# Performance work log

Hardware: AMD Instinct MI355X
Metric: run time of the kernel (lower is better)

Reference implementation:

```python
import jax, jax.numpy as jnp
import numpy as np

B, S, H, NH = 2, 2048, 2048, 16
HD = H // NH  # 128
NEG = -1e9


def _rope_tables(seq_len, dim, dtype):
    inv_freq = 1.0 / (10000.0 ** (jnp.arange(0, dim, 2, dtype=jnp.float32) / dim))
    t = jnp.arange(seq_len, dtype=jnp.float32)
    freqs = jnp.einsum('i,j->ij', t, inv_freq)          # [S, dim/2]
    emb = jnp.concatenate([freqs, freqs], axis=-1)      # [S, dim]
    return jnp.cos(emb).astype(dtype), jnp.sin(emb).astype(dtype)


def _rotate_half(x):
    x1, x2 = x[..., : x.shape[-1] // 2], x[..., x.shape[-1] // 2:]
    return jnp.concatenate([-x2, x1], axis=-1)


def setup_inputs() -> dict:
    key = jax.random.key(0)
    ks = jax.random.split(key, 5)
    hidden_states = jax.random.normal(ks[0], (B, S, H), dtype=jnp.float32)
    # causal additive mask [B, S, S]
    causal = jnp.where(jnp.tril(jnp.ones((S, S), dtype=bool)), 0.0, NEG).astype(jnp.float32)
    attention_mask = jnp.broadcast_to(causal, (B, S, S))
    sc = 1.0 / np.sqrt(H)
    Wq = jax.random.normal(ks[1], (H, H), dtype=jnp.float32) * sc
    Wk = jax.random.normal(ks[2], (H, H), dtype=jnp.float32) * sc
    Wv = jax.random.normal(ks[3], (H, H), dtype=jnp.float32) * sc
    Wo = jax.random.normal(ks[4], (H, H), dtype=jnp.float32) * sc
    return {"hidden_states": hidden_states, "attention_mask": attention_mask,
            "Wq": Wq, "Wk": Wk, "Wv": Wv, "Wo": Wo}


def reference(hidden_states, attention_mask, Wq, Wk, Wv, Wo):
    bsz, q_len, _ = hidden_states.shape
    dtype = hidden_states.dtype
    # QKV projections (nn.Linear: x @ W.T), split into heads -> [B, NH, S, HD]
    def proj(W):
        return jnp.einsum('bsh,dh->bsd', hidden_states, W).reshape(bsz, q_len, NH, HD).transpose(0, 2, 1, 3)
    q, k, v = proj(Wq), proj(Wk), proj(Wv)
    cos, sin = _rope_tables(q_len, HD, dtype)            # [S, HD]
    q = q * cos + _rotate_half(q) * sin
    k = k * cos + _rotate_half(k) * sin
    scaling = HD ** -0.5
    scores = jnp.einsum('bhqd,bhkd->bhqk', q, k) * scaling
    scores = scores + attention_mask[:, None, :, :]      # broadcast over heads
    attn = jax.nn.softmax(scores.astype(jnp.float32), axis=-1).astype(dtype)
    out = jnp.einsum('bhqk,bhkd->bhqd', attn, v)         # [B, NH, S, HD]
    out = out.transpose(0, 2, 1, 3).reshape(bsz, q_len, H)
    return jnp.einsum('bsh,dh->bsd', out, Wo)
```

## Files before the change

kernel.cpp:

```cpp
#include <hip/hip_runtime.h>
#include <hip/hip_bf16.h>
#include <math.h>

#define B_  2
#define S_  2048
#define H_  2048
#define NH_ 16
#define HD_ 128
#define M_  (B_*S_)

typedef __bf16 bf16_t;
typedef _Float16 f16_t;
typedef __bf16 bf16x8 __attribute__((ext_vector_type(8)));
typedef __bf16 bf16x4 __attribute__((ext_vector_type(4)));
typedef _Float16 f16x4 __attribute__((ext_vector_type(4)));
typedef float  f32x4  __attribute__((ext_vector_type(4)));

__device__ __forceinline__ f32x4 mfma_bf16_32(bf16x8 a, bf16x8 b, f32x4 c) {
  return __builtin_amdgcn_mfma_f32_16x16x32_bf16(a, b, c, 0, 0, 0);
}
__device__ __forceinline__ f32x4 mfma_f16_16(f16x4 a, f16x4 b, f32x4 c) {
  return __builtin_amdgcn_mfma_f32_16x16x16f16(a, b, c, 0, 0, 0);
}
__device__ __forceinline__ void gl_lds16(const void* g, void* l) {
  __builtin_amdgcn_global_load_lds((const __attribute__((address_space(1))) void*)g,
                                   (__attribute__((address_space(3))) void*)l, 16, 0, 0);
}
#define WAITCNT_VM(n) { asm volatile("" ::: "memory"); \
                        __builtin_amdgcn_s_waitcnt(((n) & 0xF) | 0x70 | 0xF00 | (((n) >> 4) << 14)); \
                        asm volatile("" ::: "memory"); }
#define BARRIER()     { asm volatile("" ::: "memory"); __builtin_amdgcn_s_barrier(); \
                        asm volatile("" ::: "memory"); }

__global__ void cvt_all(const float* __restrict__ hs, const float* __restrict__ wq,
                        const float* __restrict__ wk, const float* __restrict__ wv,
                        const float* __restrict__ wo, bf16_t* __restrict__ hs_b,
                        bf16_t* __restrict__ wqkv, bf16_t* __restrict__ wo_b) {
  int i = (blockIdx.x * 256 + threadIdx.x) * 4;
  const float* src;
  bf16_t* dst;
  if (i < 8388608)        { src = hs + i;              dst = hs_b + i; }
  else if (i < 12582912)  { src = wq + (i - 8388608);  dst = wqkv + (i - 8388608); }
  else if (i < 16777216)  { src = wk + (i - 12582912); dst = wqkv + (i - 8388608); }
  else if (i < 20971520)  { src = wv + (i - 16777216); dst = wqkv + (i - 8388608); }
  else                    { src = wo + (i - 20971520); dst = wo_b + (i - 20971520); }
  float4 v = *(const float4*)src;
  bf16x4 o;
  o[0] = (bf16_t)v.x; o[1] = (bf16_t)v.y; o[2] = (bf16_t)v.z; o[3] = (bf16_t)v.w;
  *(bf16x4*)dst = o;
}

template<int MODE>
__global__ __launch_bounds__(256, 3)
void gemm_mfma(const bf16_t* __restrict__ A, const bf16_t* __restrict__ Bt,
               bf16_t* __restrict__ outQ, bf16_t* __restrict__ outK,
               f16_t* __restrict__ outV, float* __restrict__ outF, int K) {
  __shared__ bf16_t sA[128 * 64];
  __shared__ bf16_t sB[128 * 64];
  const int tid  = threadIdx.x;
  const int lane = tid & 63;
  const int w    = tid >> 6;
  const int col  = lane & 15;
  const int quad = lane >> 4;
  const int w_m  = (w & 1) * 64;
  const int w_n  = (w >> 1) * 64;
  const int m_blk = blockIdx.y * 128;
  const int n_blk = blockIdx.x * 128;

  const int srow   = lane >> 3;
  const int schunk = (lane & 7) ^ (lane >> 3);

  const bf16_t* Abase = A  + (size_t)m_blk * K;
  const bf16_t* Bbase = Bt + (size_t)n_blk * K;

  f32x4 acc[4][4] = {};

  for (int kk = 0; kk < K; kk += 64) {
    __syncthreads();
#pragma unroll
    for (int p = 0; p < 4; ++p) {
      int seg = w * 4 + p;
      int row = seg * 8 + srow;
      gl_lds16(Abase + (size_t)row * K + kk + schunk * 8, &sA[seg * 512]);
      gl_lds16(Bbase + (size_t)row * K + kk + schunk * 8, &sB[seg * 512]);
    }
    __syncthreads();
#pragma unroll
    for (int kc = 0; kc < 2; ++kc) {
      bf16x8 af[4], bfr[4];
      const int cs = (kc * 4 + quad) ^ (col & 7);
#pragma unroll
      for (int i = 0; i < 4; ++i) {
        af[i]  = *(const bf16x8*)&sA[(w_m + i * 16 + col) * 64 + cs * 8];
        bfr[i] = *(const bf16x8*)&sB[(w_n + i * 16 + col) * 64 + cs * 8];
      }
#pragma unroll
      for (int mi = 0; mi < 4; ++mi)
#pragma unroll
        for (int ni = 0; ni < 4; ++ni)
          acc[mi][ni] = mfma_bf16_32(af[mi], bfr[ni], acc[mi][ni]);
    }
  }

  const int sel = n_blk >> 11;
  if (MODE == 0 && sel == 2) {
#pragma unroll
    for (int mi = 0; mi < 4; ++mi)
#pragma unroll
      for (int ni = 0; ni < 4; ++ni) {
        int m0 = m_blk + w_m + mi * 16 + quad * 4;
        int n  = n_blk + w_n + ni * 16 + col;
        int n_l = n & (H_ - 1);
        int head = n_l >> 7, hd = n_l & (HD_ - 1);
        int b = m0 >> 11, s0 = m0 & (S_ - 1);
        int bh = b * NH_ + head;
        int frag = (bh * 32 + (s0 >> 6)) * 32 + (hd >> 4) * 4 + ((s0 >> 4) & 3);
        int lane2 = ((s0 >> 2) & 3) * 16 + (hd & 15);
        f16x4 o;
#pragma unroll
        for (int r = 0; r < 4; ++r) o[r] = (f16_t)acc[mi][ni][r];
        *(f16x4*)&outV[(size_t)frag * 256 + lane2 * 4] = o;
      }
  } else {
#pragma unroll
    for (int mi = 0; mi < 4; ++mi)
#pragma unroll
      for (int ni = 0; ni < 4; ++ni)
#pragma unroll
        for (int r = 0; r < 4; ++r) {
          int m = m_blk + w_m + mi * 16 + quad * 4 + r;
          int n = n_blk + w_n + ni * 16 + col;
          float v = acc[mi][ni][r];
          if (MODE == 0) {
            int n_l = n & (H_ - 1);
            int head = n_l >> 7, hd = n_l & (HD_ - 1);
            int b = m >> 11, s = m & (S_ - 1);
            size_t idx = (((size_t)(b * NH_ + head)) * S_ + s) * HD_ + hd;
            if (sel == 0) outQ[idx] = (bf16_t)v;
            else          outK[idx] = (bf16_t)v;
          } else {
            outF[(size_t)m * H_ + n] = v;
          }
        }
  }
}

__global__ void rope_pack(bf16_t* __restrict__ Qb, const bf16_t* __restrict__ Kn,
                          bf16_t* __restrict__ Kp) {
  int i = blockIdx.x * 256 + threadIdx.x;
  int isK = i >> 19;
  int ii = i & 524287;
  int d8 = ii & 7;
  int s  = (ii >> 3) & (S_ - 1);
  int bh = ii >> 14;
  int d0 = d8 * 8;
  const bf16_t* row = (isK ? Kn : (const bf16_t*)Qb) + ((size_t)bh * S_ + s) * HD_;
  bf16x8 a = *(const bf16x8*)(row + d0);
  bf16x8 b = *(const bf16x8*)(row + d0 + 64);
  bf16x8 o1, o2;
#pragma unroll
  for (int j = 0; j < 8; ++j) {
    int d = d0 + j;
    float ang = (float)s * exp2f(-(float)d * (13.287712379549449f / 64.f));
    float c = cosf(ang), sn = sinf(ang);
    float x1 = (float)a[j], x2 = (float)b[j];
    o1[j] = (bf16_t)(x1 * c - x2 * sn);
    o2[j] = (bf16_t)(x2 * c + x1 * sn);
  }
  if (!isK) {
    bf16_t* wr = Qb + ((size_t)bh * S_ + s) * HD_;
    *(bf16x8*)(wr + d0)      = o1;
    *(bf16x8*)(wr + d0 + 64) = o2;
  } else {
    int kt = s >> 6, t = (s >> 4) & 3;
    int lane_ = (d8 & 3) * 16 + (s & 15);
    int kc1 = d0 >> 5;
    bf16_t* base = Kp + ((size_t)(bh * 32 + kt) * 16) * 512;
    *(bf16x8*)(base + (size_t)(t * 4 + kc1) * 512 + lane_ * 8)     = o1;
    *(bf16x8*)(base + (size_t)(t * 4 + kc1 + 2) * 512 + lane_ * 8) = o2;
  }
}

__global__ __launch_bounds__(256, 4)
void flash_attn(const bf16_t* __restrict__ Q, const bf16_t* __restrict__ Kp,
                const f16_t* __restrict__ Vp, bf16_t* __restrict__ Out) {
  __shared__ bf16_t sK[8192];
  __shared__ f16_t  sV[8192];
  const int lane = threadIdx.x & 63;
  const int col  = lane & 15;
  const int quad = lane >> 4;
  const int w    = threadIdx.x >> 6;

  const int c = blockIdx.x & 7, g = blockIdx.x >> 3;
  const int g2 = (g + (blockIdx.y >> 3)) & 3;
  const int qt = (g2 == 0) ? c : (g2 == 1) ? 15 - c : (g2 == 2) ? 16 + c : 31 - c;
  const int bh = blockIdx.y;
  const int ktmax = qt;

  const bf16_t* KpB = Kp + (size_t)bh * 32 * 8192;
  const f16_t*  VpB = Vp + (size_t)bh * 32 * 8192;

  auto stageK = [&](int kt) {
#pragma unroll
    for (int r = 0; r < 4; ++r) {
      int seg = r * 4 + w;
      gl_lds16(KpB + (size_t)kt * 8192 + seg * 512 + lane * 8, &sK[seg * 512]);
    }
  };
  auto stageV = [&](int kt) {
#pragma unroll
    for (int r = 0; r < 4; ++r) {
      int seg = r * 4 + w;
      gl_lds16(VpB + (size_t)kt * 8192 + seg * 512 + lane * 8, &sV[seg * 512]);
    }
  };

  const float scale2 = 0.12751744154f;
  const bf16_t* Qrow = Q + ((size_t)bh * S_ + qt * 64 + w * 16 + col) * HD_;
  bf16x8 qf[4];
#pragma unroll
  for (int kc = 0; kc < 4; ++kc) {
    qf[kc] = *(const bf16x8*)(Qrow + kc * 32 + quad * 8);
#pragma unroll
    for (int j = 0; j < 8; ++j) qf[kc][j] = (bf16_t)((float)qf[kc][j] * scale2);
  }

  f32x4 oacc[8] = {};
  float m_i = -1e30f, l_i = 0.f;

  stageK(0);
  stageV(0);
  WAITCNT_VM(4)
  BARRIER();

  for (int kt = 0; kt <= ktmax; ++kt) {
    f32x4 st[4] = {};
    __builtin_amdgcn_s_setprio(1);
#pragma unroll
    for (int kc = 0; kc < 4; ++kc)
#pragma unroll
      for (int t = 0; t < 4; ++t) {
        bf16x8 kf = *(const bf16x8*)&sK[(t * 4 + kc) * 512 + lane * 8];
        st[t] = mfma_bf16_32(kf, qf[kc], st[t]);
      }
    __builtin_amdgcn_s_setprio(0);

    if (kt == ktmax) {
      int ql = w * 16 + col;
#pragma unroll
      for (int t = 0; t < 4; ++t)
#pragma unroll
        for (int r = 0; r < 4; ++r)
          if (t * 16 + quad * 4 + r > ql) st[t][r] = -1e30f;
    }

    float mx = st[0][0];
#pragma unroll
    for (int t = 0; t < 4; ++t)
#pragma unroll
      for (int r = 0; r < 4; ++r) mx = fmaxf(mx, st[t][r]);
    mx = fmaxf(mx, __shfl_xor(mx, 16, 64));
    mx = fmaxf(mx, __shfl_xor(mx, 32, 64));
    if (__ballot(mx - m_i > 8.0f)) {
      float mn = fmaxf(m_i, mx);
      float alpha = exp2f(m_i - mn);
#pragma unroll
      for (int dt = 0; dt < 8; ++dt)
#pragma unroll
        for (int r = 0; r < 4; ++r) oacc[dt][r] *= alpha;
      l_i *= alpha;
      m_i = mn;
    }

    float sum = 0.f;
    f16x4 pf[4];
#pragma unroll
    for (int t = 0; t < 4; ++t)
#pragma unroll
      for (int r = 0; r < 4; ++r) {
        float pv = exp2f(st[t][r] - m_i);
        sum += pv;
        pf[t][r] = (f16_t)pv;
      }
    sum += __shfl_xor(sum, 16, 64);
    sum += __shfl_xor(sum, 32, 64);
    l_i += sum;

    WAITCNT_VM(0)
    BARRIER();

    if (kt < ktmax) stageK(kt + 1);

    __builtin_amdgcn_s_setprio(1);
#pragma unroll
    for (int t = 0; t < 4; ++t)
#pragma unroll
      for (int dt = 0; dt < 8; ++dt) {
        f16x4 vf = *(const f16x4*)&sV[(dt * 4 + t) * 256 + lane * 4];
        oacc[dt] = mfma_f16_16(vf, pf[t], oacc[dt]);
      }
    __builtin_amdgcn_s_setprio(0);

    if (kt < ktmax) {
      BARRIER();
      stageV(kt + 1);
      WAITCNT_VM(4)
      BARRIER();
    }
  }

  float inv = 1.0f / l_i;
  int b = bh >> 4, h = bh & (NH_ - 1);
  int qg = qt * 64 + w * 16 + col;
  bf16_t* Orow = Out + ((size_t)b * S_ + qg) * H_ + h * HD_;
#pragma unroll
  for (int dt = 0; dt < 8; ++dt) {
    bf16x4 o4;
#pragma unroll
    for (int r = 0; r < 4; ++r) o4[r] = (bf16_t)(oacc[dt][r] * inv);
    *(bf16x4*)(Orow + dt * 16 + quad * 4) = o4;
  }
}

extern "C" void kernel_launch(void* const* d_in, const int* in_sizes, int n_in,
                              void* d_out, int out_size, void* d_ws, size_t ws_size,
                              hipStream_t stream) {
  const float* hs = (const float*)d_in[0];
  const float* Wq = (const float*)d_in[2];
  const float* Wk = (const float*)d_in[3];
  const float* Wv = (const float*)d_in[4];
  const float* Wo = (const float*)d_in[5];
  float* out = (float*)d_out;

  char* ws = (char*)d_ws;
  size_t off = 0;
  auto alloc = [&](size_t bytes) -> void* {
    void* p = ws + off;
    off += (bytes + 255) & ~(size_t)255;
    return p;
  };
  bf16_t* hs_b  = (bf16_t*)alloc((size_t)M_ * H_ * 2);
  bf16_t* wqkv  = (bf16_t*)alloc((size_t)3 * H_ * H_ * 2);
  bf16_t* wo_b  = (bf16_t*)alloc((size_t)H_ * H_ * 2);
  bf16_t* Qbuf  = (bf16_t*)alloc((size_t)M_ * H_ * 2);
  bf16_t* Kbuf  = (bf16_t*)alloc((size_t)M_ * H_ * 2);
  f16_t*  Vp    = (f16_t*)alloc((size_t)M_ * H_ * 2);
  bf16_t* attn  = (bf16_t*)alloc((size_t)M_ * H_ * 2);

  cvt_all<<<24576, 256, 0, stream>>>(hs, Wq, Wk, Wv, Wo, hs_b, wqkv, wo_b);

  gemm_mfma<0><<<dim3(48, 32), 256, 0, stream>>>(hs_b, wqkv, Qbuf, Kbuf,
                                                 Vp, nullptr, H_);

  bf16_t* Kp = wqkv;
  rope_pack<<<4096, 256, 0, stream>>>(Qbuf, Kbuf, Kp);

  flash_attn<<<dim3(32, 32), 256, 0, stream>>>(Qbuf, Kp, Vp, attn);

  gemm_mfma<1><<<dim3(16, 32), 256, 0, stream>>>(attn, wo_b, nullptr, nullptr,
                                                 nullptr, out, H_);
}
```

Baseline: 381.3 us.

## Fuse RoPE and K packing into QKV GEMM epilogue via LDS staging

The separate rope_pack kernel is removed. The QKV GEMM epilogue for the Q and K tiles now stages its accumulators through a swizzled shared-memory tile, applies the rotary embedding, and writes Q directly and K in the packed fragment layout that flash attention expects. This drops a full read and write of Q and K through global memory and one kernel launch. In exchange the GEMM epilogue gains extra barriers and sincos work, and it reuses the tile buffer, which may affect register pressure and occupancy.

```diff
diff --git a/kernel.cpp b/kernel.cpp
--- a/kernel.cpp
+++ b/kernel.cpp
@@ -55,8 +55,9 @@
 void gemm_mfma(const bf16_t* __restrict__ A, const bf16_t* __restrict__ Bt,
                bf16_t* __restrict__ outQ, bf16_t* __restrict__ outK,
                f16_t* __restrict__ outV, float* __restrict__ outF, int K) {
-  __shared__ bf16_t sA[128 * 64];
-  __shared__ bf16_t sB[128 * 64];
+  __shared__ bf16_t sS[128 * 128];
+  bf16_t* const sA = sS;
+  bf16_t* const sB = sS + 128 * 64;
   const int tid  = threadIdx.x;
   const int lane = tid & 63;
   const int w    = tid >> 6;
@@ -121,6 +122,56 @@
         for (int r = 0; r < 4; ++r) o[r] = (f16_t)acc[mi][ni][r];
         *(f16x4*)&outV[(size_t)frag * 256 + lane2 * 4] = o;
       }
+  } else if (MODE == 0) {
+    __syncthreads();
+#pragma unroll
+    for (int mi = 0; mi < 4; ++mi)
+#pragma unroll
+      for (int ni = 0; ni < 4; ++ni) {
+        int lm0 = w_m + mi * 16 + quad * 4;
+        int ln  = w_n + ni * 16 + col;
+#pragma unroll
+        for (int r = 0; r < 4; ++r) {
+          int lm = lm0 + r;
+          sS[lm * 128 + (ln ^ ((lm & 7) << 3))] = (bf16_t)acc[mi][ni][r];
+        }
+      }
+    __syncthreads();
+    const int row  = tid >> 1;
+    const int half = tid & 1;
+    const int m    = m_blk + row;
+    const int b    = m >> 11, s = m & (S_ - 1);
+    const int head = (n_blk & (H_ - 1)) >> 7;
+    const int bh   = b * NH_ + head;
+    const int swz  = (row & 7) << 3;
+    const int kt = s >> 6, t = (s >> 4) & 3;
+    bf16_t* qwr   = outQ + ((size_t)bh * S_ + s) * HD_ + half * 32;
+    bf16_t* kbase = outK + ((size_t)(bh * 32 + kt) * 16) * 512;
+#pragma unroll
+    for (int k = 0; k < 4; ++k) {
+      int e1 = row * 128 + ((half * 32 + k * 8) ^ swz);
+      bf16x8 x1 = *(const bf16x8*)&sS[e1];
+      bf16x8 x2 = *(const bf16x8*)&sS[e1 + 64];
+      bf16x8 o1, o2;
+#pragma unroll
+      for (int j = 0; j < 8; ++j) {
+        int d = half * 32 + k * 8 + j;
+        float ang = (float)s * exp2f(-(float)d * (13.287712379549449f / 64.f));
+        float cc, sn;
+        sincosf(ang, &sn, &cc);
+        float a1 = (float)x1[j], a2 = (float)x2[j];
+        o1[j] = (bf16_t)(a1 * cc - a2 * sn);
+        o2[j] = (bf16_t)(a2 * cc + a1 * sn);
+      }
+      if (sel == 0) {
+        *(bf16x8*)(qwr + k * 8)      = o1;
+        *(bf16x8*)(qwr + 64 + k * 8) = o2;
+      } else {
+        int lane_ = k * 16 + (s & 15);
+        *(bf16x8*)(kbase + (size_t)(t * 4 + half) * 512 + lane_ * 8)     = o1;
+        *(bf16x8*)(kbase + (size_t)(t * 4 + half + 2) * 512 + lane_ * 8) = o2;
+      }
+    }
   } else {
 #pragma unroll
     for (int mi = 0; mi < 4; ++mi)
@@ -130,54 +181,8 @@
         for (int r = 0; r < 4; ++r) {
           int m = m_blk + w_m + mi * 16 + quad * 4 + r;
           int n = n_blk + w_n + ni * 16 + col;
-          float v = acc[mi][ni][r];
-          if (MODE == 0) {
-            int n_l = n & (H_ - 1);
-            int head = n_l >> 7, hd = n_l & (HD_ - 1);
-            int b = m >> 11, s = m & (S_ - 1);
-            size_t idx = (((size_t)(b * NH_ + head)) * S_ + s) * HD_ + hd;
-            if (sel == 0) outQ[idx] = (bf16_t)v;
-            else          outK[idx] = (bf16_t)v;
-          } else {
-            outF[(size_t)m * H_ + n] = v;
-          }
+          outF[(size_t)m * H_ + n] = acc[mi][ni][r];
         }
-  }
-}
-
-__global__ void rope_pack(bf16_t* __restrict__ Qb, const bf16_t* __restrict__ Kn,
-                          bf16_t* __restrict__ Kp) {
-  int i = blockIdx.x * 256 + threadIdx.x;
-  int isK = i >> 19;
-  int ii = i & 524287;
-  int d8 = ii & 7;
-  int s  = (ii >> 3) & (S_ - 1);
-  int bh = ii >> 14;
-  int d0 = d8 * 8;
-  const bf16_t* row = (isK ? Kn : (const bf16_t*)Qb) + ((size_t)bh * S_ + s) * HD_;
-  bf16x8 a = *(const bf16x8*)(row + d0);
-  bf16x8 b = *(const bf16x8*)(row + d0 + 64);
-  bf16x8 o1, o2;
-#pragma unroll
-  for (int j = 0; j < 8; ++j) {
-    int d = d0 + j;
-    float ang = (float)s * exp2f(-(float)d * (13.287712379549449f / 64.f));
-    float c = cosf(ang), sn = sinf(ang);
-    float x1 = (float)a[j], x2 = (float)b[j];
-    o1[j] = (bf16_t)(x1 * c - x2 * sn);
-    o2[j] = (bf16_t)(x2 * c + x1 * sn);
-  }
-  if (!isK) {
-    bf16_t* wr = Qb + ((size_t)bh * S_ + s) * HD_;
-    *(bf16x8*)(wr + d0)      = o1;
-    *(bf16x8*)(wr + d0 + 64) = o2;
-  } else {
-    int kt = s >> 6, t = (s >> 4) & 3;
-    int lane_ = (d8 & 3) * 16 + (s & 15);
-    int kc1 = d0 >> 5;
-    bf16_t* base = Kp + ((size_t)(bh * 32 + kt) * 16) * 512;
-    *(bf16x8*)(base + (size_t)(t * 4 + kc1) * 512 + lane_ * 8)     = o1;
-    *(bf16x8*)(base + (size_t)(t * 4 + kc1 + 2) * 512 + lane_ * 8) = o2;
   }
 }
 
@@ -343,17 +348,14 @@
   bf16_t* wqkv  = (bf16_t*)alloc((size_t)3 * H_ * H_ * 2);
   bf16_t* wo_b  = (bf16_t*)alloc((size_t)H_ * H_ * 2);
   bf16_t* Qbuf  = (bf16_t*)alloc((size_t)M_ * H_ * 2);
-  bf16_t* Kbuf  = (bf16_t*)alloc((size_t)M_ * H_ * 2);
+  bf16_t* Kp    = (bf16_t*)alloc((size_t)M_ * H_ * 2);
   f16_t*  Vp    = (f16_t*)alloc((size_t)M_ * H_ * 2);
   bf16_t* attn  = (bf16_t*)alloc((size_t)M_ * H_ * 2);
 
   cvt_all<<<24576, 256, 0, stream>>>(hs, Wq, Wk, Wv, Wo, hs_b, wqkv, wo_b);
 
-  gemm_mfma<0><<<dim3(48, 32), 256, 0, stream>>>(hs_b, wqkv, Qbuf, Kbuf,
+  gemm_mfma<0><<<dim3(48, 32), 256, 0, stream>>>(hs_b, wqkv, Qbuf, Kp,
                                                  Vp, nullptr, H_);
-
-  bf16_t* Kp = wqkv;
-  rope_pack<<<4096, 256, 0, stream>>>(Qbuf, Kbuf, Kp);
 
   flash_attn<<<dim3(32, 32), 256, 0, stream>>>(Qbuf, Kp, Vp, attn);
 
```

Result: faster. 368.1 us (-3.5%).
